# Kernel tuning notes

Hardware: AMD Instinct MI355X
Metric: run time of the kernel (lower is better)

## Reference

```python
import jax, jax.numpy as jnp
import numpy as np

CH = 512
GROUPS = 32
EPS = 1e-5
B, H, W = 4, 64, 64


def setup_inputs() -> dict:
    key = jax.random.key(0)
    ks = jax.random.split(key, 6)
    s = 1.0 / np.sqrt(CH)  # conv2d default init scale (approx, uniform fan-in)
    return {
        "x": jax.random.normal(ks[0], (B, CH, H, W), dtype=jnp.float32),
        "norm_w": jnp.ones((CH,), jnp.float32),
        "norm_b": jnp.zeros((CH,), jnp.float32),
        "q_w": jax.random.normal(ks[1], (CH, CH), jnp.float32) * s,
        "q_b": jnp.zeros((CH,), jnp.float32),
        "k_w": jax.random.normal(ks[2], (CH, CH), jnp.float32) * s,
        "k_b": jnp.zeros((CH,), jnp.float32),
        "v_w": jax.random.normal(ks[3], (CH, CH), jnp.float32) * s,
        "v_b": jnp.zeros((CH,), jnp.float32),
        "proj_w": jax.random.normal(ks[4], (CH, CH), jnp.float32) * s,
        "proj_b": jnp.zeros((CH,), jnp.float32),
    }


def _group_norm(x, w, b):
    # x: [B, C, H, W]; 32 groups over channel dim
    bsz, c, h, wd = x.shape
    xg = x.reshape(bsz, GROUPS, c // GROUPS, h, wd)
    mean = xg.mean(axis=(2, 3, 4), keepdims=True)
    var = xg.var(axis=(2, 3, 4), keepdims=True)
    xg = (xg - mean) * jax.lax.rsqrt(var + EPS)
    x = xg.reshape(bsz, c, h, wd)
    return x * w[None, :, None, None] + b[None, :, None, None]


def _conv1x1(x, w, b):
    # x: [B, C, H, W], w: [O, C] -> [B, O, H, W]
    return jnp.einsum('bchw,oc->bohw', x, w) + b[None, :, None, None]


def reference(x, norm_w, norm_b, q_w, q_b, k_w, k_b, v_w, v_b, proj_w, proj_b):
    h = _group_norm(x, norm_w, norm_b)
    b, c, hh, ww = h.shape
    n = hh * ww
    q = _conv1x1(h, q_w, q_b).reshape(b, c, n).transpose(0, 2, 1)  # [b, n, c]
    k = _conv1x1(h, k_w, k_b).reshape(b, c, n)                     # [b, c, n]
    v = _conv1x1(h, v_w, v_b).reshape(b, c, n).transpose(0, 2, 1)  # [b, n, c]
    attn = jnp.einsum('bnc,bcm->bnm', q, k) * (c ** -0.5)          # [b, n, n]
    attn = jax.nn.softmax(attn, axis=-1)
    out = jnp.einsum('bnm,bmc->bnc', attn, v)                      # [b, n, c]
    out = out.transpose(0, 2, 1).reshape(b, c, hh, ww)
    return x + _conv1x1(out, proj_w, proj_b)
```

## Files before the change

### kernel.cpp

```cpp
#include <hip/hip_runtime.h>

#define NB 4
#define CH 512
#define NPIX 4096
#define GSZ 16
#define KVB 32
#define NT (NPIX / KVB)
#define DYN_LDS 136192
#define QKV_LDS 65536

typedef __attribute__((ext_vector_type(8))) short bf16x8;
typedef __attribute__((ext_vector_type(4))) short bf16x4;
typedef __attribute__((ext_vector_type(4))) float f32x4;

#define MFMA __builtin_amdgcn_mfma_f32_16x16x32_bf16

static __device__ __forceinline__ short f2bf(float f) {
  unsigned u = __builtin_bit_cast(unsigned, f);
  u += 0x7fffu + ((u >> 16) & 1u);
  return (short)(u >> 16);
}

static __device__ __forceinline__ float bperm_f(int srclane, float v) {
  int r = __builtin_amdgcn_ds_bpermute(srclane << 2, __builtin_bit_cast(int, v));
  return __builtin_bit_cast(float, r);
}

typedef __attribute__((address_space(1))) unsigned glob_u32;
typedef __attribute__((address_space(3))) unsigned lds_u32;
static __device__ __forceinline__ void gl_lds16(const void* g, void* l) {
  __builtin_amdgcn_global_load_lds((const glob_u32*)g, (lds_u32*)l, 16, 0, 0);
}

__global__ __launch_bounds__(256) void wconv_kernel(
    const float* __restrict__ qw, const float* __restrict__ kw,
    const float* __restrict__ vw, const float* __restrict__ pw,
    short* __restrict__ wstack, short* __restrict__ wp) {
  int idx = (blockIdx.x * 256 + threadIdx.x) * 4;
  int mat = idx >> 18;
  int off = idx & 262143;
  const float* src = (mat == 0) ? qw : (mat == 1) ? kw : (mat == 2) ? vw : pw;
  short* dst = (mat < 3) ? (wstack + (size_t)mat * 262144) : wp;
  float4 v = *reinterpret_cast<const float4*>(src + off);
  bf16x4 o;
  o[0] = f2bf(v.x); o[1] = f2bf(v.y); o[2] = f2bf(v.z); o[3] = f2bf(v.w);
  *reinterpret_cast<bf16x4*>(dst + off) = o;
}

__global__ __launch_bounds__(256) void gn_kernel(
    const float* __restrict__ x, const float* __restrict__ nw,
    const float* __restrict__ nb, short* __restrict__ hT) {
  int pairid = blockIdx.x >> 1, half = blockIdx.x & 1;
  int b = pairid >> 5, g = pairid & 31;
  int tid = threadIdx.x;
  const float* base = x + (size_t)(b * CH + g * GSZ) * NPIX;
  const float4* b4 = reinterpret_cast<const float4*>(base);
  float s = 0.f, s2 = 0.f;
  for (int i = tid; i < GSZ * NPIX / 4; i += 256) {
    float4 v = b4[i];
    s += v.x + v.y + v.z + v.w;
    s2 += v.x * v.x + v.y * v.y + v.z * v.z + v.w * v.w;
  }
  #pragma unroll
  for (int m = 1; m < 64; m <<= 1) { s += __shfl_xor(s, m); s2 += __shfl_xor(s2, m); }
  __shared__ float red[8];
  if ((tid & 63) == 0) { red[(tid >> 6) * 2] = s; red[(tid >> 6) * 2 + 1] = s2; }
  __syncthreads();
  s = red[0] + red[2] + red[4] + red[6];
  s2 = red[1] + red[3] + red[5] + red[7];
  float mean = s * (1.f / 65536.f);
  float var = s2 * (1.f / 65536.f) - mean * mean;
  float rstd = rsqrtf(var + 1e-5f);
  int c = tid >> 4, nq = tid & 15;
  float wch = nw[g * GSZ + c] * rstd;
  float bch = nb[g * GSZ + c] - mean * wch;
  __shared__ short lt[GSZ][264];
  short* outb = hT + (size_t)b * NPIX * CH + g * GSZ;
  const float* srcc = base + (size_t)c * NPIX + nq * 16;
  for (int chunk = half * 8; chunk < half * 8 + 8; ++chunk) {
    const float4* sp = reinterpret_cast<const float4*>(srcc + chunk * 256);
    float4 v0 = sp[0], v1 = sp[1], v2 = sp[2], v3 = sp[3];
    bf16x8 w0, w1;
    w0[0] = f2bf(v0.x * wch + bch); w0[1] = f2bf(v0.y * wch + bch);
    w0[2] = f2bf(v0.z * wch + bch); w0[3] = f2bf(v0.w * wch + bch);
    w0[4] = f2bf(v1.x * wch + bch); w0[5] = f2bf(v1.y * wch + bch);
    w0[6] = f2bf(v1.z * wch + bch); w0[7] = f2bf(v1.w * wch + bch);
    w1[0] = f2bf(v2.x * wch + bch); w1[1] = f2bf(v2.y * wch + bch);
    w1[2] = f2bf(v2.z * wch + bch); w1[3] = f2bf(v2.w * wch + bch);
    w1[4] = f2bf(v3.x * wch + bch); w1[5] = f2bf(v3.y * wch + bch);
    w1[6] = f2bf(v3.z * wch + bch); w1[7] = f2bf(v3.w * wch + bch);
    *reinterpret_cast<bf16x8*>(&lt[c][nq * 16]) = w0;
    *reinterpret_cast<bf16x8*>(&lt[c][nq * 16 + 8]) = w1;
    __syncthreads();
    bf16x8 o0, o1;
    #pragma unroll
    for (int cc = 0; cc < 8; ++cc) o0[cc] = lt[cc][tid];
    #pragma unroll
    for (int cc = 0; cc < 8; ++cc) o1[cc] = lt[cc + 8][tid];
    short* orow = outb + (size_t)(chunk * 256 + tid) * CH;
    *reinterpret_cast<bf16x8*>(orow) = o0;
    *reinterpret_cast<bf16x8*>(orow + 8) = o1;
    __syncthreads();
  }
}

__global__ __launch_bounds__(256) void qkv_kernel(
    const short* __restrict__ wstack, const short* __restrict__ hT,
    const float* __restrict__ qb, const float* __restrict__ kb,
    const float* __restrict__ vb,
    short* __restrict__ qT, short* __restrict__ kT, short* __restrict__ vC) {
  extern __shared__ char qsm[];
  char* abuf = qsm;
  char* bbuf = qsm + 32768;

  int b = blockIdx.z;
  int by = blockIdx.y;
  int nbase = blockIdx.x * 128;
  int tid = threadIdx.x;
  int lane = tid & 63, wid = tid >> 6;
  int l15 = lane & 15, lg = lane >> 4;
  int wr = wid >> 1, wc = wid & 1;

  const short* arows = wstack + (size_t)by * 128 * CH;
  const short* brows = hT + ((size_t)b * NPIX + nbase) * CH;

  auto stage = [&](int buf, int kidx) {
    char* ad = abuf + buf * 16384;
    char* bd = bbuf + buf * 16384;
    #pragma unroll
    for (int i = 0; i < 4; ++i) {
      int off = i * 4096 + tid * 16;
      int row = off >> 7;
      int c16 = (off >> 4) & 7;
      int gchunk = (c16 ^ (row & 7)) * 8;
      gl_lds16(arows + (size_t)row * CH + kidx * 64 + gchunk, ad + off);
      gl_lds16(brows + (size_t)row * CH + kidx * 64 + gchunk, bd + off);
    }
  };

  f32x4 acc[4][4];
  #pragma unroll
  for (int mi = 0; mi < 4; ++mi)
    #pragma unroll
    for (int ni = 0; ni < 4; ++ni) acc[mi][ni] = (f32x4){0.f, 0.f, 0.f, 0.f};

  stage(0, 0);
  __syncthreads();

  int cur = 0;
  for (int kt = 0; kt < 8; ++kt) {
    if (kt + 1 < 8) stage(cur ^ 1, kt + 1);
    const char* ab = abuf + cur * 16384;
    const char* bb = bbuf + cur * 16384;
    #pragma unroll
    for (int ks = 0; ks < 2; ++ks) {
      bf16x8 af[4], bf[4];
      #pragma unroll
      for (int mi = 0; mi < 4; ++mi) {
        int row = wr * 64 + mi * 16 + l15;
        af[mi] = *reinterpret_cast<const bf16x8*>(
            ab + row * 128 + (((ks * 4 + lg) ^ (row & 7)) << 4));
      }
      #pragma unroll
      for (int ni = 0; ni < 4; ++ni) {
        int row = wc * 64 + ni * 16 + l15;
        bf[ni] = *reinterpret_cast<const bf16x8*>(
            bb + row * 128 + (((ks * 4 + lg) ^ (row & 7)) << 4));
      }
      #pragma unroll
      for (int mi = 0; mi < 4; ++mi)
        #pragma unroll
        for (int ni = 0; ni < 4; ++ni)
          acc[mi][ni] = MFMA(af[mi], bf[ni], acc[mi][ni], 0, 0, 0);
    }
    __syncthreads();
    cur ^= 1;
  }

  int oglob = by * 128;
  #pragma unroll
  for (int mi = 0; mi < 4; ++mi) {
    int oo = oglob + wr * 64 + mi * 16 + lg * 4;
    #pragma unroll
    for (int ni = 0; ni < 4; ++ni) {
      int nn = nbase + wc * 64 + ni * 16 + l15;
      f32x4 a = acc[mi][ni];
      if (oglob < 1024) {
        const float* bias = (oglob < 512) ? qb : kb;
        short* dstm = (oglob < 512) ? qT : kT;
        float sc = (oglob < 512) ? 0.044194173824159216f : 1.0f;
        int ol = oo & 511;
        bf16x4 pk;
        #pragma unroll
        for (int r = 0; r < 4; ++r) pk[r] = f2bf((a[r] + bias[ol + r]) * sc);
        *reinterpret_cast<bf16x4*>(dstm + ((size_t)b * NPIX + nn) * CH + ol) = pk;
      } else {
        int ov = oo - 1024;
        short* dstv = vC + ((size_t)b * CH + ov) * NPIX + nn;
        #pragma unroll
        for (int r = 0; r < 4; ++r) dstv[(size_t)r * NPIX] = f2bf(a[r] + vb[ov + r]);
      }
    }
  }
}

__global__ __launch_bounds__(512, 2) void flash_kernel(
    const short* __restrict__ qT, const short* __restrict__ kT,
    const short* __restrict__ vC, short* __restrict__ ao) {
  extern __shared__ char smem[];
  char* kbuf = smem;
  char* vbuf = smem + 65536;
  char* pbuf = smem + 131072;
  float* exch = (float*)(smem + 135168);

  int lin = blockIdx.y * 64 + blockIdx.x;
  int sw = (lin & 7) * 32 + (lin >> 3);
  int qb = sw & 63, b = sw >> 6;

  int tid = threadIdx.x;
  int lane = tid & 63, w = tid >> 6;
  int p = w >> 1, h = w & 1;
  int l15 = lane & 15, lg = lane >> 4;
  int qrow = qb * 64 + p * 16;

  const short* qptr = qT + ((size_t)b * NPIX + qrow + l15) * CH + lg * 8;
  bf16x8 qf[16];
  #pragma unroll
  for (int ks = 0; ks < 16; ++ks) qf[ks] = *reinterpret_cast<const bf16x8*>(qptr + ks * 32);

  f32x4 oacc[16];
  #pragma unroll
  for (int i = 0; i < 16; ++i) oacc[i] = (f32x4){0.f, 0.f, 0.f, 0.f};
  float mrow = -INFINITY, lrow = 0.f;
  bf16x8 pa_prev;
  bf16x8 vf_prev[16];
  #pragma unroll
  for (int i = 0; i < 8; ++i) pa_prev[i] = 0;
  #pragma unroll
  for (int j = 0; j < 16; ++j)
    #pragma unroll
    for (int i = 0; i < 8; ++i) vf_prev[j][i] = 0;

  const short* kTb = kT + (size_t)b * NPIX * CH;
  const short* vCb = vC + (size_t)b * CH * NPIX;
  const int swz = (l15 & 7) << 4;
  const int vswz = ((l15 >> 1) & 3) << 4;
  const int pswz = (l15 & 3) << 4;
  char* ppair = pbuf + p * 1024;
  float* exw = exch + (w * 16 + l15) * 2;
  float* exr = exch + ((w ^ 1) * 16 + l15) * 2;

  auto stage = [&](int buf, int t) {
    int m0 = t * KVB;
    char* kd = kbuf + buf * 32768;
    char* vd = vbuf + buf * 32768;
    #pragma unroll
    for (int i = 0; i < 4; ++i) {
      int r = w * 4 + i;
      const short* src = kTb + (size_t)(m0 + r) * CH + ((lane ^ (r & 7)) * 8);
      gl_lds16(src, kd + r * 1024);
    }
    #pragma unroll
    for (int i = 0; i < 4; ++i) {
      int j = w * 4 + i;
      int ch = j * 16 + (lane >> 2);
      const short* src = vCb + (size_t)ch * NPIX + m0 +
                         (((lane & 3) ^ ((lane >> 3) & 3)) * 8);
      gl_lds16(src, vd + j * 1024);
    }
  };

  stage(0, 0);
  asm volatile("s_waitcnt vmcnt(0)" ::: "memory");
  __syncthreads();

  int cur = 0;
  for (int t = 0; t < NT; ++t) {
    const char* kb_ = kbuf + cur * 32768;
    const char* vb_ = vbuf + cur * 32768;
    if (t + 1 < NT) stage(cur ^ 1, t + 1);
    f32x4 st = (f32x4){0.f, 0.f, 0.f, 0.f};
    __builtin_amdgcn_s_setprio(1);
    #pragma unroll
    for (int cs = 0; cs < 16; ++cs) {
      bf16x8 kf = *reinterpret_cast<const bf16x8*>(
          kb_ + (h * 16 + l15) * 1024 + ((cs * 64 + lg * 16) ^ swz));
      st = MFMA(kf, qf[cs], st, 0, 0, 0);
    }
    __builtin_amdgcn_s_setprio(0);
    float tmax = fmaxf(fmaxf(st[0], st[1]), fmaxf(st[2], st[3]));
    tmax = fmaxf(tmax, __shfl_xor(tmax, 16));
    tmax = fmaxf(tmax, __shfl_xor(tmax, 32));
    float pr[4];
    float psh;
    pr[0] = __expf(st[0] - tmax); pr[1] = __expf(st[1] - tmax);
    pr[2] = __expf(st[2] - tmax); pr[3] = __expf(st[3] - tmax);
    psh = (pr[0] + pr[1]) + (pr[2] + pr[3]);
    psh += __shfl_xor(psh, 16);
    psh += __shfl_xor(psh, 32);
    if (lane < 16) { exw[0] = tmax; exw[1] = psh; }
    asm volatile("s_waitcnt lgkmcnt(0)" ::: "memory");
    __builtin_amdgcn_s_barrier();
    __builtin_amdgcn_sched_barrier(0);
    float mo = exr[0], po = exr[1];
    float mnew = fmaxf(mrow, fmaxf(tmax, mo));
    float alpha = __expf(mrow - mnew);
    float scl = __expf(tmax - mnew);
    lrow = lrow * alpha + psh * scl + po * __expf(mo - mnew);
    mrow = mnew;
    {
      bf16x4 pk;
      pk[0] = f2bf(pr[0] * scl); pk[1] = f2bf(pr[1] * scl);
      pk[2] = f2bf(pr[2] * scl); pk[3] = f2bf(pr[3] * scl);
      *reinterpret_cast<bf16x4*>(ppair + l15 * 64 + ((h * 32 + lg * 8) ^ pswz)) = pk;
    }
    __builtin_amdgcn_s_setprio(1);
    #pragma unroll
    for (int j = 0; j < 16; ++j)
      oacc[j] = MFMA(pa_prev, vf_prev[j], oacc[j], 0, 0, 0);
    __builtin_amdgcn_s_setprio(0);
    if (!__all(alpha == 1.0f)) {
      float a4[4];
      #pragma unroll
      for (int r = 0; r < 4; ++r) a4[r] = bperm_f(lg * 4 + r, alpha);
      #pragma unroll
      for (int j = 0; j < 16; ++j) {
        oacc[j][0] *= a4[0]; oacc[j][1] *= a4[1];
        oacc[j][2] *= a4[2]; oacc[j][3] *= a4[3];
      }
    }
    #pragma unroll
    for (int j = 0; j < 16; ++j)
      vf_prev[j] = *reinterpret_cast<const bf16x8*>(
          vb_ + ((h * 16 + j) * 16 + l15) * 64 + ((lg * 16) ^ vswz));
    asm volatile("s_waitcnt vmcnt(0) lgkmcnt(0)" ::: "memory");
    __builtin_amdgcn_s_barrier();
    __builtin_amdgcn_sched_barrier(0);
    pa_prev = *reinterpret_cast<const bf16x8*>(ppair + l15 * 64 + ((lg * 16) ^ pswz));
    cur ^= 1;
  }
  #pragma unroll
  for (int j = 0; j < 16; ++j)
    oacc[j] = MFMA(pa_prev, vf_prev[j], oacc[j], 0, 0, 0);

  float linv = 1.f / lrow;
  float r4[4];
  #pragma unroll
  for (int r = 0; r < 4; ++r) r4[r] = bperm_f(lg * 4 + r, linv);
  short* aob = ao + ((size_t)b * NPIX + qrow) * CH;
  #pragma unroll
  for (int j = 0; j < 16; ++j) {
    int cb2 = h * 16 + j;
    #pragma unroll
    for (int r = 0; r < 4; ++r) {
      aob[(size_t)(lg * 4 + r) * CH + cb2 * 16 + l15] = f2bf(oacc[j][r] * r4[r]);
    }
  }
}

__global__ __launch_bounds__(256) void proj_kernel(
    const short* __restrict__ wpm, const short* __restrict__ ao,
    const float* __restrict__ x, const float* __restrict__ pb,
    float* __restrict__ out) {
  int b = blockIdx.z;
  int tid = threadIdx.x;
  int lane = tid & 63, wid = tid >> 6;
  int l15 = lane & 15, lg = lane >> 4;
  int ob = blockIdx.y * 64 + (wid >> 1) * 32;
  int nbase = blockIdx.x * 64 + (wid & 1) * 32;
  const short* aptr = wpm + (size_t)(ob + l15) * CH + lg * 8;
  const short* bptr = ao + ((size_t)b * NPIX + nbase + l15) * CH + lg * 8;
  f32x4 acc[2][2];
  #pragma unroll
  for (int mi = 0; mi < 2; ++mi)
    #pragma unroll
    for (int ni = 0; ni < 2; ++ni) acc[mi][ni] = (f32x4){0.f, 0.f, 0.f, 0.f};
  #pragma unroll 4
  for (int kk = 0; kk < CH; kk += 32) {
    bf16x8 a0 = *reinterpret_cast<const bf16x8*>(aptr + kk);
    bf16x8 a1 = *reinterpret_cast<const bf16x8*>(aptr + 16 * CH + kk);
    bf16x8 b0 = *reinterpret_cast<const bf16x8*>(bptr + kk);
    bf16x8 b1 = *reinterpret_cast<const bf16x8*>(bptr + 16 * CH + kk);
    acc[0][0] = MFMA(a0, b0, acc[0][0], 0, 0, 0);
    acc[0][1] = MFMA(a0, b1, acc[0][1], 0, 0, 0);
    acc[1][0] = MFMA(a1, b0, acc[1][0], 0, 0, 0);
    acc[1][1] = MFMA(a1, b1, acc[1][1], 0, 0, 0);
  }
  #pragma unroll
  for (int mi = 0; mi < 2; ++mi) {
    int oo = ob + mi * 16 + lg * 4;
    #pragma unroll
    for (int ni = 0; ni < 2; ++ni) {
      int nn = nbase + ni * 16 + l15;
      #pragma unroll
      for (int r = 0; r < 4; ++r) {
        size_t idx = ((size_t)b * CH + oo + r) * NPIX + nn;
        out[idx] = acc[mi][ni][r] + pb[oo + r] + x[idx];
      }
    }
  }
}

extern "C" void kernel_launch(void* const* d_in, const int* in_sizes, int n_in,
                              void* d_out, int out_size, void* d_ws, size_t ws_size,
                              hipStream_t stream) {
  const float* x  = (const float*)d_in[0];
  const float* nw = (const float*)d_in[1];
  const float* nb = (const float*)d_in[2];
  const float* qw = (const float*)d_in[3];
  const float* qb = (const float*)d_in[4];
  const float* kw = (const float*)d_in[5];
  const float* kb = (const float*)d_in[6];
  const float* vw = (const float*)d_in[7];
  const float* vb = (const float*)d_in[8];
  const float* pw = (const float*)d_in[9];
  const float* pb = (const float*)d_in[10];
  char* ws = (char*)d_ws;
  short* wstack = (short*)(ws);
  short* wp     = (short*)(ws + 1572864);
  short* hT     = (short*)(ws + 2101248);
  short* qT     = (short*)(ws + 18878464);
  short* kT     = (short*)(ws + 35655680);
  short* vC     = (short*)(ws + 52432896);
  short* ao     = hT;
  float* out = (float*)d_out;

  hipFuncSetAttribute((const void*)flash_kernel,
                      hipFuncAttributeMaxDynamicSharedMemorySize, DYN_LDS);
  hipFuncSetAttribute((const void*)qkv_kernel,
                      hipFuncAttributeMaxDynamicSharedMemorySize, QKV_LDS);

  wconv_kernel<<<1024, 256, 0, stream>>>(qw, kw, vw, pw, wstack, wp);
  gn_kernel<<<256, 256, 0, stream>>>(x, nw, nb, hT);
  qkv_kernel<<<dim3(32, 12, NB), 256, QKV_LDS, stream>>>(wstack, hT, qb, kb, vb, qT, kT, vC);
  flash_kernel<<<dim3(64, NB), 512, DYN_LDS, stream>>>(qT, kT, vC, ao);
  proj_kernel<<<dim3(64, 8, NB), 256, 0, stream>>>(wp, ao, x, pb, out);
}
```

Baseline: 471.6 us.

## Tile proj GEMM through LDS with 128x128 blocks and split QK accumulation

The projection GEMM moves from direct global loads with 64x64 tiles to a double-buffered, swizzled LDS-staged 128x128 tile scheme, the same one the QKV kernel uses. This should cut redundant global traffic and raise MFMA density per wave. In the flash kernel the QK^T reduction now alternates between two accumulators, which shortens the dependent MFMA chain. The new proj tiling launches fewer blocks, which may reduce occupancy.

```diff
diff --git a/kernel.cpp b/kernel.cpp
--- a/kernel.cpp
+++ b/kernel.cpp
@@ -7,7 +7,7 @@
 #define KVB 32
 #define NT (NPIX / KVB)
 #define DYN_LDS 136192
-#define QKV_LDS 65536
+#define GEMM_LDS 65536
 
 typedef __attribute__((ext_vector_type(8))) short bf16x8;
 typedef __attribute__((ext_vector_type(4))) short bf16x4;
@@ -180,10 +180,10 @@
   int oglob = by * 128;
   #pragma unroll
   for (int mi = 0; mi < 4; ++mi) {
-    int oo = oglob + wr * 64 + mi * 16 + lg * 4;
+    int oo = oglob + (wid >> 1) * 64 + mi * 16 + lg * 4;
     #pragma unroll
     for (int ni = 0; ni < 4; ++ni) {
-      int nn = nbase + wc * 64 + ni * 16 + l15;
+      int nn = nbase + (wid & 1) * 64 + ni * 16 + l15;
       f32x4 a = acc[mi][ni];
       if (oglob < 1024) {
         const float* bias = (oglob < 512) ? qb : kb;
@@ -279,15 +279,20 @@
     const char* kb_ = kbuf + cur * 32768;
     const char* vb_ = vbuf + cur * 32768;
     if (t + 1 < NT) stage(cur ^ 1, t + 1);
-    f32x4 st = (f32x4){0.f, 0.f, 0.f, 0.f};
+    f32x4 sa = (f32x4){0.f, 0.f, 0.f, 0.f};
+    f32x4 sb = (f32x4){0.f, 0.f, 0.f, 0.f};
     __builtin_amdgcn_s_setprio(1);
     #pragma unroll
-    for (int cs = 0; cs < 16; ++cs) {
-      bf16x8 kf = *reinterpret_cast<const bf16x8*>(
+    for (int cs = 0; cs < 16; cs += 2) {
+      bf16x8 kf0 = *reinterpret_cast<const bf16x8*>(
           kb_ + (h * 16 + l15) * 1024 + ((cs * 64 + lg * 16) ^ swz));
-      st = MFMA(kf, qf[cs], st, 0, 0, 0);
+      bf16x8 kf1 = *reinterpret_cast<const bf16x8*>(
+          kb_ + (h * 16 + l15) * 1024 + (((cs + 1) * 64 + lg * 16) ^ swz));
+      sa = MFMA(kf0, qf[cs], sa, 0, 0, 0);
+      sb = MFMA(kf1, qf[cs + 1], sb, 0, 0, 0);
     }
     __builtin_amdgcn_s_setprio(0);
+    f32x4 st = sa + sb;
     float tmax = fmaxf(fmaxf(st[0], st[1]), fmaxf(st[2], st[3]));
     tmax = fmaxf(tmax, __shfl_xor(tmax, 16));
     tmax = fmaxf(tmax, __shfl_xor(tmax, 32));
@@ -362,40 +367,85 @@
     const short* __restrict__ wpm, const short* __restrict__ ao,
     const float* __restrict__ x, const float* __restrict__ pb,
     float* __restrict__ out) {
+  extern __shared__ char qsm[];
+  char* abuf = qsm;
+  char* bbuf = qsm + 32768;
+
   int b = blockIdx.z;
+  int by = blockIdx.y;
+  int nbase = blockIdx.x * 128;
   int tid = threadIdx.x;
   int lane = tid & 63, wid = tid >> 6;
   int l15 = lane & 15, lg = lane >> 4;
-  int ob = blockIdx.y * 64 + (wid >> 1) * 32;
-  int nbase = blockIdx.x * 64 + (wid & 1) * 32;
-  const short* aptr = wpm + (size_t)(ob + l15) * CH + lg * 8;
-  const short* bptr = ao + ((size_t)b * NPIX + nbase + l15) * CH + lg * 8;
-  f32x4 acc[2][2];
-  #pragma unroll
-  for (int mi = 0; mi < 2; ++mi)
-    #pragma unroll
-    for (int ni = 0; ni < 2; ++ni) acc[mi][ni] = (f32x4){0.f, 0.f, 0.f, 0.f};
-  #pragma unroll 4
-  for (int kk = 0; kk < CH; kk += 32) {
-    bf16x8 a0 = *reinterpret_cast<const bf16x8*>(aptr + kk);
-    bf16x8 a1 = *reinterpret_cast<const bf16x8*>(aptr + 16 * CH + kk);
-    bf16x8 b0 = *reinterpret_cast<const bf16x8*>(bptr + kk);
-    bf16x8 b1 = *reinterpret_cast<const bf16x8*>(bptr + 16 * CH + kk);
-    acc[0][0] = MFMA(a0, b0, acc[0][0], 0, 0, 0);
-    acc[0][1] = MFMA(a0, b1, acc[0][1], 0, 0, 0);
-    acc[1][0] = MFMA(a1, b0, acc[1][0], 0, 0, 0);
-    acc[1][1] = MFMA(a1, b1, acc[1][1], 0, 0, 0);
-  }
-  #pragma unroll
-  for (int mi = 0; mi < 2; ++mi) {
-    int oo = ob + mi * 16 + lg * 4;
-    #pragma unroll
-    for (int ni = 0; ni < 2; ++ni) {
-      int nn = nbase + ni * 16 + l15;
+  int wr = wid >> 1, wc = wid & 1;
+
+  const short* arows = wpm + (size_t)by * 128 * CH;
+  const short* brows = ao + ((size_t)b * NPIX + nbase) * CH;
+
+  auto stage = [&](int buf, int kidx) {
+    char* ad = abuf + buf * 16384;
+    char* bd = bbuf + buf * 16384;
+    #pragma unroll
+    for (int i = 0; i < 4; ++i) {
+      int off = i * 4096 + tid * 16;
+      int row = off >> 7;
+      int c16 = (off >> 4) & 7;
+      int gchunk = (c16 ^ (row & 7)) * 8;
+      gl_lds16(arows + (size_t)row * CH + kidx * 64 + gchunk, ad + off);
+      gl_lds16(brows + (size_t)row * CH + kidx * 64 + gchunk, bd + off);
+    }
+  };
+
+  f32x4 acc[4][4];
+  #pragma unroll
+  for (int mi = 0; mi < 4; ++mi)
+    #pragma unroll
+    for (int ni = 0; ni < 4; ++ni) acc[mi][ni] = (f32x4){0.f, 0.f, 0.f, 0.f};
+
+  stage(0, 0);
+  __syncthreads();
+
+  int cur = 0;
+  for (int kt = 0; kt < 8; ++kt) {
+    if (kt + 1 < 8) stage(cur ^ 1, kt + 1);
+    const char* ab = abuf + cur * 16384;
+    const char* bb = bbuf + cur * 16384;
+    #pragma unroll
+    for (int ks = 0; ks < 2; ++ks) {
+      bf16x8 af[4], bf[4];
+      #pragma unroll
+      for (int mi = 0; mi < 4; ++mi) {
+        int row = wr * 64 + mi * 16 + l15;
+        af[mi] = *reinterpret_cast<const bf16x8*>(
+            ab + row * 128 + (((ks * 4 + lg) ^ (row & 7)) << 4));
+      }
+      #pragma unroll
+      for (int ni = 0; ni < 4; ++ni) {
+        int row = wc * 64 + ni * 16 + l15;
+        bf[ni] = *reinterpret_cast<const bf16x8*>(
+            bb + row * 128 + (((ks * 4 + lg) ^ (row & 7)) << 4));
+      }
+      #pragma unroll
+      for (int mi = 0; mi < 4; ++mi)
+        #pragma unroll
+        for (int ni = 0; ni < 4; ++ni)
+          acc[mi][ni] = MFMA(af[mi], bf[ni], acc[mi][ni], 0, 0, 0);
+    }
+    __syncthreads();
+    cur ^= 1;
+  }
+
+  #pragma unroll
+  for (int mi = 0; mi < 4; ++mi) {
+    int oo = by * 128 + wr * 64 + mi * 16 + lg * 4;
+    #pragma unroll
+    for (int ni = 0; ni < 4; ++ni) {
+      int nn = nbase + wc * 64 + ni * 16 + l15;
+      f32x4 a = acc[mi][ni];
       #pragma unroll
       for (int r = 0; r < 4; ++r) {
         size_t idx = ((size_t)b * CH + oo + r) * NPIX + nn;
-        out[idx] = acc[mi][ni][r] + pb[oo + r] + x[idx];
+        out[idx] = a[r] + pb[oo + r] + x[idx];
       }
     }
   }
@@ -428,11 +478,13 @@
   hipFuncSetAttribute((const void*)flash_kernel,
                       hipFuncAttributeMaxDynamicSharedMemorySize, DYN_LDS);
   hipFuncSetAttribute((const void*)qkv_kernel,
-                      hipFuncAttributeMaxDynamicSharedMemorySize, QKV_LDS);
+                      hipFuncAttributeMaxDynamicSharedMemorySize, GEMM_LDS);
+  hipFuncSetAttribute((const void*)proj_kernel,
+                      hipFuncAttributeMaxDynamicSharedMemorySize, GEMM_LDS);
 
   wconv_kernel<<<1024, 256, 0, stream>>>(qw, kw, vw, pw, wstack, wp);
   gn_kernel<<<256, 256, 0, stream>>>(x, nw, nb, hT);
-  qkv_kernel<<<dim3(32, 12, NB), 256, QKV_LDS, stream>>>(wstack, hT, qb, kb, vb, qT, kT, vC);
+  qkv_kernel<<<dim3(32, 12, NB), 256, GEMM_LDS, stream>>>(wstack, hT, qb, kb, vb, qT, kT, vC);
   flash_kernel<<<dim3(64, NB), 512, DYN_LDS, stream>>>(qT, kT, vC, ao);
-  proj_kernel<<<dim3(64, 8, NB), 256, 0, stream>>>(wp, ao, x, pb, out);
-}
+  proj_kernel<<<dim3(32, 4, NB), 256, GEMM_LDS, stream>>>(wp, ao, x, pb, out);
+}
```

Measured after the change: 435.1 us. 1.08x faster.
